# Optimization experiments

Measured on AMD Instinct MI355X. Metric: run time of the kernel, lower is better.

The kernel has to match this reference:

```python
import jax, jax.numpy as jnp
import numpy as np

TEMPERATURE = 0.07
NEG_RATIO = 1.0
ADJ_DENSITY = 0.002
SAMPLE_SEED = 42


def setup_inputs() -> dict:
    key = jax.random.key(0)
    k1, k2, k3 = jax.random.split(key, 3)
    I, E, D = 4096, 16384, 64
    item = jax.random.normal(k1, (I, D), dtype=jnp.float32)
    ent = jax.random.normal(k2, (E, D), dtype=jnp.float32)
    # sparse binary adjacency: ~33 positives per item on average
    adj = (jax.random.uniform(k3, (I, E)) < ADJ_DENSITY).astype(jnp.int32)
    return {"item_embeddings": item, "entity_embeddings": ent, "adj_matrix": adj}


def reference(item_embeddings, entity_embeddings, adj_matrix):
    # L2-normalize rows, cosine similarity / temperature
    it = item_embeddings / jnp.linalg.norm(item_embeddings, axis=1, keepdims=True)
    en = entity_embeddings / jnp.linalg.norm(entity_embeddings, axis=1, keepdims=True)
    sim = jnp.einsum('id,ed->ie', it, en) / TEMPERATURE  # [I, E]

    pos_mask = adj_matrix > 0                             # [I, E]
    neg_mask = ~pos_mask
    num_pos = pos_mask.sum(axis=1)                        # [I]
    num_neg = neg_mask.sum(axis=1)
    # num_negatives = min(int(num_pos * ratio), num_neg)  (per item)
    k = jnp.minimum(jnp.floor(num_pos.astype(jnp.float32) * NEG_RATIO).astype(jnp.int32), num_neg)

    # negative sampling without replacement: uniform keys, take k smallest among negatives
    u = jax.random.uniform(jax.random.key(SAMPLE_SEED), sim.shape)
    u = jnp.where(pos_mask, jnp.inf, u)                   # positives rank last
    rank = jnp.argsort(jnp.argsort(u, axis=1), axis=1)    # per-row rank of each entity
    samp = (rank < k[:, None]) & neg_mask                 # sampled negatives [I, E]

    valid = (num_pos > 0) & (k > 0)                       # items contributing pairs

    # stable per-item logsumexp over sampled negatives
    neg_logits = jnp.where(samp, sim, -jnp.inf)
    m = jnp.max(neg_logits, axis=1)                       # [I], -inf if no sampled negs
    m_safe = jnp.where(valid, m, 0.0)
    S = jnp.sum(jnp.where(samp, jnp.exp(sim - m_safe[:, None]), 0.0), axis=1)  # [I]

    # per positive pair: CE with pos as class 0 over [pos, sampled_negs]
    # loss = log(exp(pos) + sum exp(neg)) - pos, stabilized with pairwise max
    pm = jnp.maximum(sim, m_safe[:, None])
    loss_pair = jnp.log(jnp.exp(sim - pm) + S[:, None] * jnp.exp(m_safe[:, None] - pm)) + pm - sim

    pair_mask = pos_mask & valid[:, None]
    total = jnp.sum(jnp.where(pair_mask, loss_pair, 0.0))
    n_pairs = jnp.sum(jnp.where(valid, num_pos, 0))
    return jnp.where(n_pairs > 0, total / jnp.maximum(n_pairs, 1).astype(jnp.float32), 0.0)
```

## Files before the change

### kernel.cpp

```cpp
#include <hip/hip_runtime.h>
#include <math.h>


constexpr int D      = 64;
constexpr int PCAP   = 96;
constexpr int CCAP   = 192;
constexpr int SELCAP = 128;

typedef int int4v __attribute__((ext_vector_type(4)));

__device__ __forceinline__ void threefry2x32(unsigned x0, unsigned x1,
                                             unsigned& o0, unsigned& o1) {
  const unsigned ks0 = 0u;
  const unsigned ks1 = 42u;
  const unsigned ks2 = 0x1BD11BDAu ^ 0u ^ 42u;
  x0 += ks0; x1 += ks1;
#define TF_R(r) { x0 += x1; x1 = (x1 << (r)) | (x1 >> (32 - (r))); x1 ^= x0; }
  TF_R(13) TF_R(15) TF_R(26) TF_R(6)
  x0 += ks1; x1 += ks2 + 1u;
  TF_R(17) TF_R(29) TF_R(16) TF_R(24)
  x0 += ks2; x1 += ks0 + 2u;
  TF_R(13) TF_R(15) TF_R(26) TF_R(6)
  x0 += ks0; x1 += ks1 + 3u;
  TF_R(17) TF_R(29) TF_R(16) TF_R(24)
  x0 += ks1; x1 += ks2 + 4u;
  TF_R(13) TF_R(15) TF_R(26) TF_R(6)
  x0 += ks2; x1 += ks0 + 5u;
#undef TF_R
  o0 = x0; o1 = x1;
}

__device__ __forceinline__ int lane_prior(unsigned long long m) {
  return (int)__builtin_amdgcn_mbcnt_hi(
      (unsigned)(m >> 32), __builtin_amdgcn_mbcnt_lo((unsigned)m, 0u));
}

__device__ __forceinline__ void wave_append(bool pred, int e,
                                            int* cnt, int* list, int cap) {
  unsigned long long m = __ballot(pred);
  if (m) {
    const int lane = threadIdx.x & 63;
    const int leader = __builtin_ctzll(m);
    int base = 0;
    if (lane == leader) base = atomicAdd(cnt, (int)__popcll(m));
    base = __builtin_amdgcn_readlane(base, leader);
    if (pred) {
      int s = base + lane_prior(m);
      if (s < cap) list[s] = e;
    }
  }
}

__device__ __forceinline__ void wave_append2(bool pred, int e, unsigned key,
                                             int* cnt, int* li, unsigned* lk,
                                             int cap) {
  unsigned long long m = __ballot(pred);
  if (m) {
    const int lane = threadIdx.x & 63;
    const int leader = __builtin_ctzll(m);
    int base = 0;
    if (lane == leader) base = atomicAdd(cnt, (int)__popcll(m));
    base = __builtin_amdgcn_readlane(base, leader);
    if (pred) {
      int s = base + lane_prior(m);
      if (s < cap) { li[s] = e; lk[s] = key; }
    }
  }
}

__device__ __forceinline__ float dot_sim(const float* __restrict__ ent, int e,
                                         const float* itemn) {
  const float4* er = (const float4*)(ent + ((size_t)e << 6));
  float dot = 0.f, ss = 0.f;
#pragma unroll
  for (int q = 0; q < 16; ++q) {
    float4 f = er[q];
    dot += itemn[4 * q + 0] * f.x + itemn[4 * q + 1] * f.y +
           itemn[4 * q + 2] * f.z + itemn[4 * q + 3] * f.w;
    ss += f.x * f.x + f.y * f.y + f.z * f.z + f.w * f.w;
  }
  return dot * (1.0f / sqrtf(ss));
}

__device__ __forceinline__ float block_max(float v, float* wred, int t) {
#pragma unroll
  for (int off = 32; off; off >>= 1) v = fmaxf(v, __shfl_xor(v, off, 64));
  __syncthreads();
  if ((t & 63) == 0) wred[t >> 6] = v;
  __syncthreads();
  return fmaxf(fmaxf(wred[0], wred[1]), fmaxf(wred[2], wred[3]));
}

__device__ __forceinline__ float block_sum(float v, float* wred, int t) {
#pragma unroll
  for (int off = 32; off; off >>= 1) v += __shfl_xor(v, off, 64);
  __syncthreads();
  if ((t & 63) == 0) wred[t >> 6] = v;
  __syncthreads();
  return wred[0] + wred[1] + wred[2] + wred[3];
}

template <bool WSOUT>
__global__ __launch_bounds__(256) void infonce_mono(
    const float* __restrict__ item, const float* __restrict__ ent,
    const int* __restrict__ adj, int I, int E,
    float* __restrict__ loss, int* __restrict__ cnt,
    double* __restrict__ accum, int* __restrict__ paircnt) {
  const int t = threadIdx.x;
  const int halfI = I >> 1;
  const int iA = blockIdx.x;
  const int iB = iA + halfI;
  const unsigned HALF = (unsigned)halfI * (unsigned)E;
  const unsigned baseA = (unsigned)iA * (unsigned)E;

  __shared__ int s_pos[2][PCAP];
  __shared__ int s_ci[2][CCAP];
  __shared__ unsigned s_ck[2][CCAP];
  __shared__ int s_sel[SELCAP];
  __shared__ int s_hist[256];
  __shared__ float s_itemn[D];
  __shared__ float s_wred[4];
  __shared__ int s_np[2], s_nc[2];
  __shared__ int s_nsel, s_bbin, s_cbef, s_fnc;
  __shared__ float s_scale;

  if (t < 2) { s_np[t] = 0; s_nc[t] = 0; }
  __syncthreads();

  const int nvec = E >> 2;
  const int4v* adjA = (const int4v*)(adj + (size_t)iA * E);
  const int4v* adjB = (const int4v*)(adj + (size_t)iB * E);
  for (int v = t; v < nvec; v += 256) {
    int4v a4 = __builtin_nontemporal_load(&adjA[v]);
    int4v b4 = __builtin_nontemporal_load(&adjB[v]);
    const unsigned e0 = (unsigned)v * 4u;
    unsigned o0[4], o1[4];
#pragma unroll
    for (int c = 0; c < 4; ++c) {
      const unsigned x = baseA + e0 + c;
      threefry2x32(x, x + HALF, o0[c], o1[c]);
    }
    unsigned pmA = 0, pmB = 0, cmA = 0, cmB = 0;
#pragma unroll
    for (int c = 0; c < 4; ++c) {
      const bool pa = (a4[c] > 0), pb = (b4[c] > 0);
      pmA |= pa ? (1u << c) : 0u;
      pmB |= pb ? (1u << c) : 0u;
      cmA |= (!pa && (o0[c] >> 24) == 0u) ? (1u << c) : 0u;
      cmB |= (!pb && (o1[c] >> 24) == 0u) ? (1u << c) : 0u;
    }
    if (__ballot(pmA != 0)) {
#pragma unroll
      for (int c = 0; c < 4; ++c)
        if (pmA & (1u << c)) {
          int s = atomicAdd(&s_np[0], 1);
          if (s < PCAP) s_pos[0][s] = (int)(e0 + c);
        }
    }
    if (__ballot(pmB != 0)) {
#pragma unroll
      for (int c = 0; c < 4; ++c)
        if (pmB & (1u << c)) {
          int s = atomicAdd(&s_np[1], 1);
          if (s < PCAP) s_pos[1][s] = (int)(e0 + c);
        }
    }
    if (__ballot(cmA != 0)) {
#pragma unroll
      for (int c = 0; c < 4; ++c)
        if (cmA & (1u << c)) {
          int s = atomicAdd(&s_nc[0], 1);
          if (s < CCAP) { s_ci[0][s] = (int)(e0 + c); s_ck[0][s] = o0[c] >> 9; }
        }
    }
    if (__ballot(cmB != 0)) {
#pragma unroll
      for (int c = 0; c < 4; ++c)
        if (cmB & (1u << c)) {
          int s = atomicAdd(&s_nc[1], 1);
          if (s < CCAP) { s_ci[1][s] = (int)(e0 + c); s_ck[1][s] = o1[c] >> 9; }
        }
    }
  }
  __syncthreads();

  for (int r2 = 0; r2 < 2; ++r2) {
    const int row = r2 ? iB : iA;
    const int npos = min(s_np[r2], PCAP);
    const int k = min(npos, E - npos);
    const bool valid = (npos > 0 && k > 0);
    float rowloss = 0.f;
    if (valid) {
      if (t == 0) s_nsel = 0;
      __syncthreads();
      int ncand = min(s_nc[r2], CCAP);
      int rneed = k;
      if (s_nc[r2] > CCAP || ncand < k) {
        s_hist[t] = 0;
        if (t == 0) s_fnc = 0;
        __syncthreads();
        const int* adjR = adj + (size_t)row * E;
        for (int e = t; e < E; e += 256) {
          if (adjR[e] > 0) continue;
          unsigned o0, o1;
          threefry2x32(baseA + (unsigned)e, baseA + (unsigned)e + HALF, o0, o1);
          atomicAdd(&s_hist[(r2 ? o1 : o0) >> 24], 1);
        }
        __syncthreads();
        if (t == 0) {
          int cum = 0, b = 0;
          while (b < 255 && cum + s_hist[b] < k) { cum += s_hist[b]; ++b; }
          s_bbin = b; s_cbef = cum;
        }
        __syncthreads();
        const int b = s_bbin;
        for (int e = t; e < E; e += 256) {
          bool neg = (adjR[e] <= 0);
          unsigned o0, o1, bits = 0xFFFFFFFFu;
          if (neg) {
            threefry2x32(baseA + (unsigned)e, baseA + (unsigned)e + HALF, o0, o1);
            bits = r2 ? o1 : o0;
          }
          int b8 = (int)(bits >> 24);
          wave_append(neg && b8 < b, e, &s_nsel, s_sel, SELCAP);
          wave_append2(neg && b8 == b, e, bits >> 9,
                       &s_fnc, s_ci[r2], s_ck[r2], CCAP);
        }
        __syncthreads();
        ncand = min(s_fnc, CCAP);
        rneed = k - s_cbef;
      }

      for (int i = t; i < ncand; i += 256) {
        const unsigned mk = s_ck[r2][i];
        const int mi = s_ci[r2][i];
        int rank = 0;
        for (int c = 0; c < ncand; ++c) {
          const unsigned ck = s_ck[r2][c];
          const int ci = s_ci[r2][c];
          rank += (ck < mk || (ck == mk && ci < mi)) ? 1 : 0;
        }
        if (rank < rneed) {
          int s = atomicAdd(&s_nsel, 1);
          if (s < SELCAP) s_sel[s] = mi;
        }
      }

      float iv = 0.f;
      if (t < D) iv = item[(size_t)row * D + t];
      if (t < 64) {
        float ss = iv * iv;
#pragma unroll
        for (int off = 32; off; off >>= 1) ss += __shfl_xor(ss, off, 64);
        if (t == 0) s_scale = (1.0f / sqrtf(ss)) * (1.0f / 0.07f);
      }
      __syncthreads();
      if (t < D) s_itemn[t] = iv * s_scale;
      __syncthreads();
      const int nsel = min(s_nsel, SELCAP);

      float myv = (t < nsel) ? dot_sim(ent, s_sel[t], s_itemn) : -INFINITY;
      const float m = block_max(myv, s_wred, t);
      float v2 = (t < nsel) ? expf(myv - m) : 0.f;
      const float S = block_sum(v2, s_wred, t);

      float lp = 0.f;
      if (t < npos) {
        float sp = dot_sim(ent, s_pos[r2][t], s_itemn);
        float pm = fmaxf(sp, m);
        lp = logf(expf(sp - pm) + S * expf(m - pm)) + pm - sp;
      }
      rowloss = block_sum(lp, s_wred, t);
    }
    if (WSOUT) {
      if (t == 0) { loss[row] = valid ? rowloss : 0.f; cnt[row] = valid ? npos : 0; }
    } else {
      if (valid && t == 0) {
        atomicAdd(accum, (double)rowloss);
        atomicAdd(paircnt, npos);
      }
    }
    __syncthreads();
  }
}

__global__ __launch_bounds__(256) void reduce_out(
    const float* __restrict__ loss, const int* __restrict__ cnt, int I,
    float* __restrict__ out) {
  const int t = threadIdx.x;
  __shared__ double s_l[256];
  __shared__ int s_n[256];
  double l = 0.0;
  int n = 0;
  for (int i = t; i < I; i += 256) { l += (double)loss[i]; n += cnt[i]; }
  s_l[t] = l; s_n[t] = n;
  __syncthreads();
  for (int off = 128; off; off >>= 1) {
    if (t < off) { s_l[t] += s_l[t + off]; s_n[t] += s_n[t + off]; }
    __syncthreads();
  }
  if (t == 0) out[0] = (s_n[0] > 0) ? (float)(s_l[0] / (double)s_n[0]) : 0.f;
}

__global__ void infonce_init(double* accum, int* cnt) {
  if (threadIdx.x == 0 && blockIdx.x == 0) { accum[0] = 0.0; cnt[0] = 0; }
}

__global__ void infonce_final(const double* __restrict__ accum,
                              const int* __restrict__ cnt,
                              float* __restrict__ out) {
  if (threadIdx.x == 0 && blockIdx.x == 0) {
    int n = cnt[0];
    out[0] = (n > 0) ? (float)(accum[0] / (double)n) : 0.f;
  }
}

extern "C" void kernel_launch(void* const* d_in, const int* in_sizes, int n_in,
                              void* d_out, int out_size, void* d_ws, size_t ws_size,
                              hipStream_t stream) {
  const float* item = (const float*)d_in[0];
  const float* ent  = (const float*)d_in[1];
  const int*   adj  = (const int*)d_in[2];
  const int I = in_sizes[0] / D;
  const int E = in_sizes[1] / D;

  const size_t need = (size_t)I * 8;
  if (ws_size >= need && (I % 2) == 0) {
    float* lossb = (float*)d_ws;
    int*   cntb  = (int*)(lossb + I);
    infonce_mono<true><<<I / 2, 256, 0, stream>>>(item, ent, adj, I, E,
                                                  lossb, cntb, nullptr, nullptr);
    reduce_out<<<1, 256, 0, stream>>>(lossb, cntb, I, (float*)d_out);
  } else {
    double* accum   = (double*)d_ws;
    int*    paircnt = (int*)((char*)d_ws + 8);
    infonce_init<<<1, 64, 0, stream>>>(accum, paircnt);
    infonce_mono<false><<<I / 2, 256, 0, stream>>>(item, ent, adj, I, E,
                                                   nullptr, nullptr, accum, paircnt);
    infonce_final<<<1, 64, 0, stream>>>(accum, paircnt, (float*)d_out);
  }
}
```

Baseline: 153.3 us.

## Pack candidate key/index into u64, split rank and dot work across lane pairs

Candidate keys and entity indices are packed into one 64-bit shared-memory word, so each rank comparison is a single 64-bit compare and one shared load. The O(n^2) rank count and the 64-wide dot products are each split across two lanes and combined with a shuffle, halving per-thread serial work. In the fallback path, positives are now rescanned from the adjacency row rather than read from the capped list. This adds shuffles and a costlier fallback in exchange for shorter per-thread latency in the candidate ranking and similarity stages.

```diff
diff --git a/kernel.cpp b/kernel.cpp
--- a/kernel.cpp
+++ b/kernel.cpp
@@ -8,6 +8,7 @@
 constexpr int SELCAP = 128;
 
 typedef int int4v __attribute__((ext_vector_type(4)));
+typedef unsigned long long u64;
 
 __device__ __forceinline__ void threefry2x32(unsigned x0, unsigned x1,
                                              unsigned& o0, unsigned& o1) {
@@ -50,10 +51,8 @@
     }
   }
 }
-
-__device__ __forceinline__ void wave_append2(bool pred, int e, unsigned key,
-                                             int* cnt, int* li, unsigned* lk,
-                                             int cap) {
+__device__ __forceinline__ void wave_append_pack(bool pred, u64 pack,
+                                                 int* cnt, u64* lst, int cap) {
   unsigned long long m = __ballot(pred);
   if (m) {
     const int lane = threadIdx.x & 63;
@@ -63,7 +62,7 @@
     base = __builtin_amdgcn_readlane(base, leader);
     if (pred) {
       int s = base + lane_prior(m);
-      if (s < cap) { li[s] = e; lk[s] = key; }
+      if (s < cap) lst[s] = pack;
     }
   }
 }
@@ -114,8 +113,7 @@
   const unsigned baseA = (unsigned)iA * (unsigned)E;
 
   __shared__ int s_pos[2][PCAP];
-  __shared__ int s_ci[2][CCAP];
-  __shared__ unsigned s_ck[2][CCAP];
+  __shared__ u64 s_cpack[2][CCAP];
   __shared__ int s_sel[SELCAP];
   __shared__ int s_hist[256];
   __shared__ float s_itemn[D];
@@ -170,7 +168,8 @@
       for (int c = 0; c < 4; ++c)
         if (cmA & (1u << c)) {
           int s = atomicAdd(&s_nc[0], 1);
-          if (s < CCAP) { s_ci[0][s] = (int)(e0 + c); s_ck[0][s] = o0[c] >> 9; }
+          if (s < CCAP)
+            s_cpack[0][s] = ((u64)(o0[c] >> 9) << 32) | (e0 + c);
         }
     }
     if (__ballot(cmB != 0)) {
@@ -178,24 +177,28 @@
       for (int c = 0; c < 4; ++c)
         if (cmB & (1u << c)) {
           int s = atomicAdd(&s_nc[1], 1);
-          if (s < CCAP) { s_ci[1][s] = (int)(e0 + c); s_ck[1][s] = o1[c] >> 9; }
-        }
-    }
-  }
-  __syncthreads();
-
+          if (s < CCAP)
+            s_cpack[1][s] = ((u64)(o1[c] >> 9) << 32) | (e0 + c);
+        }
+    }
+  }
+  __syncthreads();
+
+  const int g = t >> 1, l = t & 1;
   for (int r2 = 0; r2 < 2; ++r2) {
     const int row = r2 ? iB : iA;
     const int npos = min(s_np[r2], PCAP);
     const int k = min(npos, E - npos);
     const bool valid = (npos > 0 && k > 0);
     float rowloss = 0.f;
+    bool fb = false;
     if (valid) {
       if (t == 0) s_nsel = 0;
       __syncthreads();
       int ncand = min(s_nc[r2], CCAP);
       int rneed = k;
-      if (s_nc[r2] > CCAP || ncand < k) {
+      fb = (s_nc[r2] > CCAP) || (ncand < k);
+      if (fb) {
         s_hist[t] = 0;
         if (t == 0) s_fnc = 0;
         __syncthreads();
@@ -223,26 +226,24 @@
           }
           int b8 = (int)(bits >> 24);
           wave_append(neg && b8 < b, e, &s_nsel, s_sel, SELCAP);
-          wave_append2(neg && b8 == b, e, bits >> 9,
-                       &s_fnc, s_ci[r2], s_ck[r2], CCAP);
+          wave_append_pack(neg && b8 == b,
+                           ((u64)(bits >> 9) << 32) | (unsigned)e,
+                           &s_fnc, s_cpack[r2], CCAP);
         }
         __syncthreads();
         ncand = min(s_fnc, CCAP);
         rneed = k - s_cbef;
       }
 
-      for (int i = t; i < ncand; i += 256) {
-        const unsigned mk = s_ck[r2][i];
-        const int mi = s_ci[r2][i];
+      for (int i = g; i < ncand; i += 128) {
+        const u64 my = s_cpack[r2][i];
         int rank = 0;
-        for (int c = 0; c < ncand; ++c) {
-          const unsigned ck = s_ck[r2][c];
-          const int ci = s_ci[r2][c];
-          rank += (ck < mk || (ck == mk && ci < mi)) ? 1 : 0;
-        }
-        if (rank < rneed) {
+        for (int c = l; c < ncand; c += 2)
+          rank += (s_cpack[r2][c] < my) ? 1 : 0;
+        rank += __shfl_xor(rank, 1, 64);
+        if (l == 0 && rank < rneed) {
           int s = atomicAdd(&s_nsel, 1);
-          if (s < SELCAP) s_sel[s] = mi;
+          if (s < SELCAP) s_sel[s] = (int)(unsigned)(my & 0xFFFFFFFFull);
         }
       }
 
@@ -259,16 +260,56 @@
       __syncthreads();
       const int nsel = min(s_nsel, SELCAP);
 
-      float myv = (t < nsel) ? dot_sim(ent, s_sel[t], s_itemn) : -INFINITY;
-      const float m = block_max(myv, s_wred, t);
-      float v2 = (t < nsel) ? expf(myv - m) : 0.f;
+      float sim = -INFINITY;
+      {
+        float dot = 0.f, ss = 0.f;
+        if (g < nsel) {
+          const float4* er = (const float4*)(ent + ((size_t)s_sel[g] << 6));
+#pragma unroll
+          for (int q = 0; q < 8; ++q) {
+            float4 f = er[l * 8 + q];
+            const float* w = &s_itemn[32 * l + 4 * q];
+            dot += w[0] * f.x + w[1] * f.y + w[2] * f.z + w[3] * f.w;
+            ss += f.x * f.x + f.y * f.y + f.z * f.z + f.w * f.w;
+          }
+        }
+        dot += __shfl_xor(dot, 1, 64);
+        ss += __shfl_xor(ss, 1, 64);
+        if (g < nsel && l == 0) sim = dot * (1.0f / sqrtf(ss));
+      }
+      const float m = block_max(sim, s_wred, t);
+      float v2 = (sim != -INFINITY) ? expf(sim - m) : 0.f;
       const float S = block_sum(v2, s_wred, t);
 
       float lp = 0.f;
-      if (t < npos) {
-        float sp = dot_sim(ent, s_pos[r2][t], s_itemn);
-        float pm = fmaxf(sp, m);
-        lp = logf(expf(sp - pm) + S * expf(m - pm)) + pm - sp;
+      if (!fb) {
+        float dot = 0.f, ss = 0.f;
+        if (g < npos) {
+          const float4* er = (const float4*)(ent + ((size_t)s_pos[r2][g] << 6));
+#pragma unroll
+          for (int q = 0; q < 8; ++q) {
+            float4 f = er[l * 8 + q];
+            const float* w = &s_itemn[32 * l + 4 * q];
+            dot += w[0] * f.x + w[1] * f.y + w[2] * f.z + w[3] * f.w;
+            ss += f.x * f.x + f.y * f.y + f.z * f.z + f.w * f.w;
+          }
+        }
+        dot += __shfl_xor(dot, 1, 64);
+        ss += __shfl_xor(ss, 1, 64);
+        if (g < npos && l == 0) {
+          float sp = dot * (1.0f / sqrtf(ss));
+          float pm = fmaxf(sp, m);
+          lp = logf(expf(sp - pm) + S * expf(m - pm)) + pm - sp;
+        }
+      } else {
+        const int* adjR = adj + (size_t)row * E;
+        for (int e = t; e < E; e += 256) {
+          if (adjR[e] > 0) {
+            float sp = dot_sim(ent, e, s_itemn);
+            float pm = fmaxf(sp, m);
+            lp += logf(expf(sp - pm) + S * expf(m - pm)) + pm - sp;
+          }
+        }
       }
       rowloss = block_sum(lp, s_wred, t);
     }
```

Measured after the change: 167.6 us. +9.4%, slower.
